# Kernel optimization log

Measured on AMD Instinct MI355X. Metric: run time of the kernel, lower is better.

Reference implementation:

```python
import jax, jax.numpy as jnp
import numpy as np

K = 3            # kernel_size
KK = K * K       # 9 neighbors per pixel
DILATIONS = [1, 2, 3]
NUM_HEADS = 3


def conv2d(x, w, b, dilation, padding):
    # x: [B,Cin,H,W], w: [Cout,Cin,kh,kw]
    out = jax.lax.conv_general_dilated(
        x, w, window_strides=(1, 1),
        padding=((padding, padding), (padding, padding)),
        rhs_dilation=(dilation, dilation),
        dimension_numbers=('NCHW', 'OIHW', 'NCHW'))
    if b is not None:
        out = out + b[None, :, None, None]
    return out


def unfold3(x, dil):
    # nn.Unfold(kernel=3, dilation=dil, padding=dil, stride=1): [B,C,H,W] -> [B, C*9, H*W]
    B, C, H, W = x.shape
    xp = jnp.pad(x, ((0, 0), (0, 0), (dil, dil), (dil, dil)))
    patches = [xp[:, :, i * dil:i * dil + H, j * dil:j * dil + W]
               for i in range(K) for j in range(K)]
    p = jnp.stack(patches, axis=2)          # [B,C,9,H,W] (channel-major like torch unfold)
    return p.reshape(B, C * KK, H * W)


def bilinear_sample(x, py, px):
    # x: [B,C,H,W]; py, px: [B,K2,H,W] float sample coords -> [B,C,K2,H,W]
    B, C, H, W = x.shape
    K2 = py.shape[1]
    y0 = jnp.floor(py); x0 = jnp.floor(px)
    wy = py - y0; wx = px - x0
    x_flat = x.reshape(B, C, H * W)

    def gather(yi, xi):
        yii = yi.astype(jnp.int32); xii = xi.astype(jnp.int32)
        valid = (yii >= 0) & (yii < H) & (xii >= 0) & (xii < W)
        yc = jnp.clip(yii, 0, H - 1); xc = jnp.clip(xii, 0, W - 1)
        idx = (yc * W + xc).reshape(B, -1)                       # [B, K2*H*W]
        vals = jnp.take_along_axis(x_flat, idx[:, None, :], axis=2)
        vals = vals.reshape(B, C, K2, H, W)
        return vals * valid[:, None].astype(x.dtype)

    v00 = gather(y0, x0); v01 = gather(y0, x0 + 1)
    v10 = gather(y0 + 1, x0); v11 = gather(y0 + 1, x0 + 1)
    wy = wy[:, None]; wx = wx[:, None]
    return (v00 * (1 - wy) * (1 - wx) + v01 * (1 - wy) * wx
            + v10 * wy * (1 - wx) + v11 * wy * wx)


def deform_conv(x, offsets, w, b, dil):
    # torchvision DeformConv2d, stride 1, padding=dil, dilation=dil, kernel 3
    B, C, H, W = x.shape
    off = offsets.reshape(B, KK, 2, H, W)                 # [..., (dy,dx), ...]
    ky, kx = jnp.meshgrid(jnp.arange(K), jnp.arange(K), indexing='ij')
    base_dy = (ky.reshape(KK) * dil - dil).astype(x.dtype)
    base_dx = (kx.reshape(KK) * dil - dil).astype(x.dtype)
    hh = jnp.arange(H, dtype=x.dtype); ww = jnp.arange(W, dtype=x.dtype)
    py = hh[None, None, :, None] + base_dy[None, :, None, None] + off[:, :, 0]
    px = ww[None, None, None, :] + base_dx[None, :, None, None] + off[:, :, 1]
    sampled = bilinear_sample(x, py, px)                  # [B,C,9,H,W]
    out = jnp.einsum('bckhw,ock->bohw', sampled, w.reshape(w.shape[0], C, KK))
    return out + b[None, :, None, None]


def adda_attention(q, k, v, head_dim, dil, deform_params):
    # q,k,v: [B,d,H,W] (already stop-gradiented)
    B, d, H, W = q.shape
    scale = head_dim ** -0.5
    if dil != 1:
        ow, ob, dw, db = deform_params
        offsets = conv2d(k, ow, ob, dil, dil)             # [B, 2*9, H, W]
        k = deform_conv(k, offsets, dw, db, dil)
        v = deform_conv(v, offsets, dw, db, dil)
    ku = unfold3(k, dil)                                  # [B, d*9, HW]
    vu = unfold3(v, dil)
    g = d // head_dim
    HW = H * W
    qh = q.reshape(B, g, head_dim, 1, HW).transpose(0, 1, 4, 3, 2)   # [B,g,HW,1,hd]
    kh = ku.reshape(B, g, head_dim, KK, HW).transpose(0, 1, 4, 2, 3) # [B,g,HW,hd,9]
    vh = vu.reshape(B, g, head_dim, KK, HW).transpose(0, 1, 4, 3, 2) # [B,g,HW,9,hd]
    attn = jax.nn.softmax((qh @ kh) * scale, axis=-1)                # [B,g,HW,1,9]
    o = attn @ vh                                                    # [B,g,HW,1,hd]
    return o.transpose(0, 2, 1, 3, 4).reshape(B, H, W, d)


def setup_inputs() -> dict:
    key = jax.random.key(0)
    ks = jax.random.split(key, 16)
    B, H, W, C = 8, 64, 64, 192
    hd = C // NUM_HEADS  # 64 == C // num_dilation
    inp = {
        'x': jax.random.normal(ks[0], (B, H, W, C), jnp.float32),
        'qkv_w': jax.random.normal(ks[1], (3 * C, C, 1, 1), jnp.float32) * 0.05,
        'proj_w': jax.random.normal(ks[2], (C, C), jnp.float32) * 0.05,
        'proj_b': jnp.zeros((C,), jnp.float32),
        'off_w2': jax.random.normal(ks[3], (2 * KK, hd, K, K), jnp.float32) * 0.01,
        'off_b2': jnp.zeros((2 * KK,), jnp.float32),
        'def_w2': jax.random.normal(ks[4], (hd, hd, K, K), jnp.float32) * 0.05,
        'def_b2': jnp.zeros((hd,), jnp.float32),
        'off_w3': jax.random.normal(ks[5], (2 * KK, hd, K, K), jnp.float32) * 0.01,
        'off_b3': jnp.zeros((2 * KK,), jnp.float32),
        'def_w3': jax.random.normal(ks[6], (hd, hd, K, K), jnp.float32) * 0.05,
        'def_b3': jnp.zeros((hd,), jnp.float32),
    }
    return inp


def reference(x, qkv_w, proj_w, proj_b,
              off_w2, off_b2, def_w2, def_b2,
              off_w3, off_b3, def_w3, def_b3):
    B, H, W, C = x.shape
    nd = len(DILATIONS)
    d = C // nd
    hd = C // NUM_HEADS
    xc = x.transpose(0, 3, 1, 2)                              # [B,C,H,W]
    qkv = conv2d(xc, qkv_w, None, 1, 0)                       # [B,3C,H,W]
    qkv = qkv.reshape(B, 3, nd, d, H, W).transpose(2, 1, 0, 3, 4, 5)  # [nd,3,B,d,H,W]
    qkv = jax.lax.stop_gradient(qkv)                          # q,k,v are .detach()'d in torch
    deform = {2: (off_w2, off_b2, def_w2, def_b2),
              3: (off_w3, off_b3, def_w3, def_b3)}
    outs = []
    for i, dil in enumerate(DILATIONS):
        outs.append(adda_attention(qkv[i, 0], qkv[i, 1], qkv[i, 2],
                                   hd, dil, deform.get(dil)))
    out = jnp.stack(outs, axis=3).reshape(B, H, W, C)         # permute(1,2,3,0,4).reshape
    return out @ proj_w.T + proj_b
```

## Files before the change

kernel.cpp:

```cpp
#include <hip/hip_runtime.h>
#include <cmath>

#define kB    8
#define kH    64
#define kW    64
#define kHW   4096
#define kC    192
#define kD    64
#define kM    (kB * kHW)
#define kNQKV 576

typedef unsigned short ushort_t;
typedef __attribute__((ext_vector_type(8))) short  s8v;
typedef __attribute__((ext_vector_type(4))) float  f4v;

__device__ inline unsigned short bf16r(float f) {
    union { float f; unsigned u; } v; v.f = f;
    unsigned u = v.u + 0x7FFFu + ((v.u >> 16) & 1u);
    return (unsigned short)(u >> 16);
}
__device__ inline float bfu(short s) {
    union { unsigned u; float f; } v;
    v.u = ((unsigned)(unsigned short)s) << 16;
    return v.f;
}

__global__ void cvt_bf16(const float* __restrict__ src, unsigned* __restrict__ dst, int n2) {
    int i = blockIdx.x * 256 + threadIdx.x;
    if (i >= n2) return;
    float2 f = ((const float2*)src)[i];
    dst[i] = (unsigned)bf16r(f.x) | ((unsigned)bf16r(f.y) << 16);
}

__global__ void prep_all(const float* __restrict__ qkv_w,
                         const float* __restrict__ proj_w,
                         const float* __restrict__ def_w2,
                         const float* __restrict__ def_w3,
                         const float* __restrict__ off_w2,
                         const float* __restrict__ off_w3,
                         ushort_t* __restrict__ awb,
                         ushort_t* __restrict__ pwbp,
                         ushort_t* __restrict__ dwtb2,
                         ushort_t* __restrict__ dwtb3,
                         ushort_t* __restrict__ owtb2,
                         ushort_t* __restrict__ owtb3) {
    const int bid = blockIdx.x;
    const int tid = threadIdx.x;
    if (bid < 54) {
        int idx = bid * 256 + tid;
        if (idx >= 36 * 6 * 64) return;
        int lane = idx & 63;
        int kc   = (idx >> 6) % 6;
        int s    = idx / 384;
        int row  = s * 16 + (lane & 15);
        int k0   = kc * 32 + (lane >> 4) * 8;
        const float* src = qkv_w + (size_t)row * kC + k0;
        ushort_t* dst = awb + (size_t)idx * 8;
#pragma unroll
        for (int j = 0; j < 8; ++j) dst[j] = bf16r(src[j]);
    } else if (bid < 72) {
        int idx = (bid - 54) * 256 + tid;
        if (idx >= 12 * 6 * 64) return;
        int lane = idx & 63;
        int kc   = (idx >> 6) % 6;
        int s    = idx / 384;
        int row  = s * 16 + (lane & 15);
        int k0   = kc * 32 + (lane >> 4) * 8;
        const float* src = proj_w + (size_t)row * kC + k0;
        ushort_t* dst = pwbp + (size_t)idx * 8;
#pragma unroll
        for (int j = 0; j < 8; ++j) dst[j] = bf16r(src[j]);
    } else if (bid < 360) {
        const float* dw = (bid < 216) ? def_w2 : def_w3;
        ushort_t* dwtb  = (bid < 216) ? dwtb2 : dwtb3;
        int l = ((bid < 216) ? (bid - 72) : (bid - 216)) * 256 + tid;
        if (l >= kD * kD * 9) return;
        int o = l / 576;
        int c = (l / 9) % 64;
        int kk = l % 9;
        dwtb[(kk * 64 + o) * 64 + c] = bf16r(dw[l]);
    } else {
        const float* ow = (bid < 432) ? off_w2 : off_w3;
        ushort_t* owtb  = (bid < 432) ? owtb2 : owtb3;
        int l = ((bid < 432) ? (bid - 360) : (bid - 432)) * 256 + tid;
        if (l >= 9 * 32 * 64) return;
        int kk = l >> 11;
        int j  = (l >> 6) & 31;
        int c  = l & 63;
        owtb[l] = (j < 18) ? bf16r(ow[j * 576 + c * 9 + kk]) : (ushort_t)0;
    }
}

__global__ __launch_bounds__(256) void qkv_mfma3(const ushort_t* __restrict__ xb,
                                                 const ushort_t* __restrict__ awb,
                                                 ushort_t* __restrict__ qkvpx) {
    __shared__ ushort_t xs[64 * kC];

    const int tid = threadIdx.x;
    const int bx  = blockIdx.x;
    const int lb  = (bx & 7) * 64 + (bx >> 3);
    const int m0  = lb * 64;
    const int ty3 = blockIdx.y;

#pragma unroll
    for (int i = 0; i < 6; ++i) {
        int il = i * 256 + tid;
        int p  = il / 24;
        int cc = il % 24;
        uint4 v = *(const uint4*)(xb + (size_t)(m0 + p) * kC + cc * 8);
        int dst = p * 384 + ((cc * 16) ^ ((p & 7) << 4));
        *(uint4*)((char*)xs + dst) = v;
    }
    __syncthreads();

    const int lane = tid & 63;
    const int wave = tid >> 6;
    const int l15  = lane & 15;
    const int q    = lane >> 4;
    const int sbase = ty3 * 12 + wave * 3;

    f4v acc[3][4];
#pragma unroll
    for (int i = 0; i < 3; ++i)
#pragma unroll
        for (int m = 0; m < 4; ++m) acc[i][m] = (f4v){0.f, 0.f, 0.f, 0.f};

    const ushort_t* ap = awb + ((size_t)sbase * 6 * 64 + lane) * 8;

#pragma unroll
    for (int kc = 0; kc < 6; ++kc) {
        s8v bfr[4];
#pragma unroll
        for (int m = 0; m < 4; ++m) {
            int row = m * 16 + l15;
            int col = (kc * 64 + q * 16) ^ ((l15 & 7) << 4);
            bfr[m] = *(const s8v*)((const char*)xs + row * 384 + col);
        }
#pragma unroll
        for (int i = 0; i < 3; ++i) {
            s8v a = *(const s8v*)(ap + (size_t)(i * 6 + kc) * 64 * 8);
#pragma unroll
            for (int m = 0; m < 4; ++m)
                acc[i][m] = __builtin_amdgcn_mfma_f32_16x16x32_bf16(a, bfr[m], acc[i][m], 0, 0, 0);
        }
    }

#pragma unroll
    for (int i = 0; i < 3; ++i) {
        int s   = sbase + i;
        int ty  = s >> 2;
        int c64 = (s & 3) * 16 + q * 4;
        ushort_t* obase = qkvpx + (size_t)ty * kM * 64 + (size_t)m0 * 64 + c64;
#pragma unroll
        for (int m = 0; m < 4; ++m) {
            f4v v = acc[i][m];
            uint2 u;
            u.x = (unsigned)bf16r(v.x) | ((unsigned)bf16r(v.y) << 16);
            u.y = (unsigned)bf16r(v.z) | ((unsigned)bf16r(v.w) << 16);
            *(uint2*)(obase + (size_t)(m * 16 + l15) * 64) = u;
        }
    }
}

__global__ __launch_bounds__(256) void off_conv_mfma(const ushort_t* __restrict__ kpx,
                                                     const ushort_t* __restrict__ owtb,
                                                     const float* __restrict__ obias,
                                                     float* __restrict__ offb,
                                                     int dil) {
    const int lb = (blockIdx.x & 7) * 64 + (blockIdx.x >> 3);
    const int b = lb >> 6;
    const int y = lb & 63;
    const int tid  = threadIdx.x;
    const int lane = tid & 63;
    const int wave = tid >> 6;
    const int l15  = lane & 15;
    const int q    = lane >> 4;
    const int px   = wave * 16 + l15;

    const ushort_t* inpx = kpx + (size_t)b * kHW * 64 + q * 8;

    f4v acc[2];
    acc[0] = (f4v){0.f, 0.f, 0.f, 0.f};
    acc[1] = (f4v){0.f, 0.f, 0.f, 0.f};

#pragma unroll
    for (int kk = 0; kk < 9; ++kk) {
        const int yy = y + (kk / 3 - 1) * dil;
        const int xx = px + (kk % 3 - 1) * dil;
        const bool valid = (yy >= 0) & (yy < kH) & (xx >= 0) & (xx < kW);
        const size_t idx = valid ? (size_t)(yy * kW + xx) * 64 : 0;
        s8v a0 = *(const s8v*)(inpx + idx);
        s8v a1 = *(const s8v*)(inpx + idx + 32);
        if (!valid) {
            a0 = (s8v){0, 0, 0, 0, 0, 0, 0, 0};
            a1 = (s8v){0, 0, 0, 0, 0, 0, 0, 0};
        }
        const ushort_t* wb = owtb + (size_t)kk * 2048 + l15 * 64 + q * 8;
#pragma unroll
        for (int nbk = 0; nbk < 2; ++nbk) {
            s8v b0 = *(const s8v*)(wb + nbk * 1024);
            s8v b1 = *(const s8v*)(wb + nbk * 1024 + 32);
            acc[nbk] = __builtin_amdgcn_mfma_f32_16x16x32_bf16(a0, b0, acc[nbk], 0, 0, 0);
            acc[nbk] = __builtin_amdgcn_mfma_f32_16x16x32_bf16(a1, b1, acc[nbk], 0, 0, 0);
        }
    }
#pragma unroll
    for (int nbk = 0; nbk < 2; ++nbk) {
        int n = nbk * 16 + l15;
        if (n < 18) {
            float bias = obias[n];
            f4v v = acc[nbk];
            v.x += bias; v.y += bias; v.z += bias; v.w += bias;
            *(f4v*)&offb[((size_t)b * 18 + n) * kHW + y * kW + wave * 16 + q * 4] = v;
        }
    }
}

template<int DIL>
__global__ __launch_bounds__(512) void deform_lds(const ushort_t* __restrict__ kpx,
                                                  const ushort_t* __restrict__ vpx,
                                                  const float* __restrict__ offb,
                                                  const ushort_t* __restrict__ dwtb,
                                                  const float* __restrict__ db,
                                                  ushort_t* __restrict__ outkpx,
                                                  ushort_t* __restrict__ outvpx) {
    constexpr int NR = 2 * DIL + 4;
    __shared__ ushort_t kv[NR * 4096];
    __shared__ ushort_t wlds[9 * 4096];

    const int tid = threadIdx.x;
    const int bx  = blockIdx.x;
    const int lb  = (bx & 7) * 64 + (bx >> 3);
    const int t   = lb >> 8;
    const int b   = (lb >> 5) & 7;
    const int y0  = (lb & 31) * 2;
    const int wlo = y0 - DIL - 1;

    const ushort_t* inb = (t ? vpx : kpx) + (size_t)b * kHW * 64;
    ushort_t* outp = t ? outvpx : outkpx;

#pragma unroll
    for (int i = 0; i < 9; ++i) {
        int g = (i * 512 + tid) * 16;
        uint4 v = *(const uint4*)((const char*)dwtb + g);
        int row = (g >> 7) & 63;
        int dst = g ^ ((row & 7) << 4);
        *(uint4*)((char*)wlds + dst) = v;
    }
#pragma unroll
    for (int r = 0; r < NR; ++r) {
        int gy = min(max(wlo + r, 0), kH - 1);
        uint4 v = *(const uint4*)(inb + (size_t)gy * 4096 + tid * 8);
        int x  = tid >> 3;
        int cc = tid & 7;
        int dst = r * 8192 + ((x * 128 + cc * 16) ^ ((x & 7) << 4));
        *(uint4*)((char*)kv + dst) = v;
    }
    __syncthreads();

    const int lane = tid & 63;
    const int wave = tid >> 6;
    const int ry   = wave >> 2;
    const int wc   = wave & 3;
    const int l15  = lane & 15;
    const int q    = lane >> 4;
    const int y    = y0 + ry;
    const int px   = wc * 16 + l15;
    const int wsw  = (l15 & 7) << 4;
    const int wcol0 = (q * 16) ^ wsw;
    const int wcol1 = (q * 16 + 64) ^ wsw;

    const ushort_t* inpx = inb + q * 8;

    f4v acc[4];
#pragma unroll
    for (int ob = 0; ob < 4; ++ob) acc[ob] = (f4v){0.f, 0.f, 0.f, 0.f};

    const float* offrow = offb + (size_t)b * 18 * kHW + y * kW + px;
    float offv[18];
#pragma unroll
    for (int i = 0; i < 18; ++i) offv[i] = offrow[(size_t)i * kHW];

#pragma unroll
    for (int kk = 0; kk < 9; ++kk) {
        float oy = offv[kk * 2 + 0];
        float ox = offv[kk * 2 + 1];
        float py  = (float)y  + (float)((kk / 3 - 1) * DIL) + oy;
        float pxf = (float)px + (float)((kk % 3 - 1) * DIL) + ox;
        float fy = floorf(py), fx = floorf(pxf);
        float wy = py - fy, wx = pxf - fx;
        int iy0 = (int)fy, ix0 = (int)fx;
        int iy1 = iy0 + 1, ix1 = ix0 + 1;
        int y0c = min(max(iy0, 0), kH - 1), x0c = min(max(ix0, 0), kW - 1);
        int y1c = min(max(iy1, 0), kH - 1), x1c = min(max(ix1, 0), kW - 1);
        bool vy0 = (iy0 >= 0) & (iy0 < kH), vx0 = (ix0 >= 0) & (ix0 < kW);
        bool vy1 = (iy1 >= 0) & (iy1 < kH), vx1 = (ix1 >= 0) & (ix1 < kW);
        float w0 = (vy0 && vx0) ? (1.f - wy) * (1.f - wx) : 0.f;
        float w1 = (vy0 && vx1) ? (1.f - wy) * wx : 0.f;
        float w2 = (vy1 && vx0) ? wy * (1.f - wx) : 0.f;
        float w3 = (vy1 && vx1) ? wy * wx : 0.f;

        s8v c[8];
        if (__builtin_expect(fabsf(oy) < 1.0f, 1)) {
            int r0 = min(max(y0c - wlo, 0), NR - 1);
            int r1 = min(max(y1c - wlo, 0), NR - 1);
            int b00 = r0 * 8192 + ((x0c * 128 + q * 16) ^ ((x0c & 7) << 4));
            int b00h = r0 * 8192 + ((x0c * 128 + q * 16 + 64) ^ ((x0c & 7) << 4));
            int b01 = r0 * 8192 + ((x1c * 128 + q * 16) ^ ((x1c & 7) << 4));
            int b01h = r0 * 8192 + ((x1c * 128 + q * 16 + 64) ^ ((x1c & 7) << 4));
            int b10 = r1 * 8192 + ((x0c * 128 + q * 16) ^ ((x0c & 7) << 4));
            int b10h = r1 * 8192 + ((x0c * 128 + q * 16 + 64) ^ ((x0c & 7) << 4));
            int b11 = r1 * 8192 + ((x1c * 128 + q * 16) ^ ((x1c & 7) << 4));
            int b11h = r1 * 8192 + ((x1c * 128 + q * 16 + 64) ^ ((x1c & 7) << 4));
            c[0] = *(const s8v*)((const char*)kv + b00);
            c[1] = *(const s8v*)((const char*)kv + b00h);
            c[2] = *(const s8v*)((const char*)kv + b01);
            c[3] = *(const s8v*)((const char*)kv + b01h);
            c[4] = *(const s8v*)((const char*)kv + b10);
            c[5] = *(const s8v*)((const char*)kv + b10h);
            c[6] = *(const s8v*)((const char*)kv + b11);
            c[7] = *(const s8v*)((const char*)kv + b11h);
        } else {
            size_t i00 = (size_t)(y0c * kW + x0c) * 64;
            size_t i01 = (size_t)(y0c * kW + x1c) * 64;
            size_t i10 = (size_t)(y1c * kW + x0c) * 64;
            size_t i11 = (size_t)(y1c * kW + x1c) * 64;
            c[0] = *(const s8v*)(inpx + i00);
            c[1] = *(const s8v*)(inpx + i00 + 32);
            c[2] = *(const s8v*)(inpx + i01);
            c[3] = *(const s8v*)(inpx + i01 + 32);
            c[4] = *(const s8v*)(inpx + i10);
            c[5] = *(const s8v*)(inpx + i10 + 32);
            c[6] = *(const s8v*)(inpx + i11);
            c[7] = *(const s8v*)(inpx + i11 + 32);
        }

        s8v b0, b1;
#pragma unroll
        for (int j = 0; j < 8; ++j) {
            float v0 = w0 * bfu(c[0][j]) + w1 * bfu(c[2][j]) +
                       w2 * bfu(c[4][j]) + w3 * bfu(c[6][j]);
            float v1 = w0 * bfu(c[1][j]) + w1 * bfu(c[3][j]) +
                       w2 * bfu(c[5][j]) + w3 * bfu(c[7][j]);
            b0[j] = (short)bf16r(v0);
            b1[j] = (short)bf16r(v1);
        }
        const char* wkk = (const char*)wlds + kk * 8192 + l15 * 128;
#pragma unroll
        for (int obb = 0; obb < 4; ++obb) {
            s8v a0w = *(const s8v*)(wkk + obb * 2048 + wcol0);
            s8v a1w = *(const s8v*)(wkk + obb * 2048 + wcol1);
            acc[obb] = __builtin_amdgcn_mfma_f32_16x16x32_bf16(a0w, b0, acc[obb], 0, 0, 0);
            acc[obb] = __builtin_amdgcn_mfma_f32_16x16x32_bf16(a1w, b1, acc[obb], 0, 0, 0);
        }
    }

    ushort_t* orow = outp + ((size_t)b * kHW + y * kW + px) * 64 + q * 4;
#pragma unroll
    for (int obb = 0; obb < 4; ++obb) {
        float4 bias = *(const float4*)&db[obb * 16 + q * 4];
        f4v v = acc[obb];
        uint2 u;
        u.x = (unsigned)bf16r(v.x + bias.x) | ((unsigned)bf16r(v.y + bias.y) << 16);
        u.y = (unsigned)bf16r(v.z + bias.z) | ((unsigned)bf16r(v.w + bias.w) << 16);
        *(uint2*)(orow + obb * 16) = u;
    }
}

__global__ __launch_bounds__(256) void attn_px(const ushort_t* __restrict__ qpx,
                                               const ushort_t* __restrict__ kpx,
                                               const ushort_t* __restrict__ vpx,
                                               ushort_t* __restrict__ aopx,
                                               int branch, int dil) {
    const int lb = (blockIdx.x & 7) * 128 + (blockIdx.x >> 3);
    const int b    = lb >> 7;
    const int y    = (lb >> 1) & 63;
    const int half = lb & 1;
    const int tid  = threadIdx.x;
    const int wave = tid >> 6;
    const int l    = tid & 63;
    const int pxq  = l >> 3;
    const int cg   = l & 7;
    const int x = half * 32 + wave * 8 + pxq;
    const int p = y * kW + x;
    const size_t pbase = (size_t)b * kHW;

    const ushort_t* qb = qpx + (pbase + p) * 64 + cg * 8;
    s8v q0 = *(const s8v*)qb;
    float qf[8];
#pragma unroll
    for (int j = 0; j < 8; ++j) qf[j] = bfu(q0[j]);

    int offs[9]; float msk[9];
#pragma unroll
    for (int kk = 0; kk < 9; ++kk) {
        int dy = (kk / 3 - 1) * dil, dx = (kk % 3 - 1) * dil;
        int yy = y + dy, xx = x + dx;
        bool v = (yy >= 0) & (yy < kH) & (xx >= 0) & (xx < kW);
        offs[kk] = v ? (p + dy * kW + dx) : p;
        msk[kk] = v ? 1.f : 0.f;
    }
    float e[9];
#pragma unroll
    for (int kk = 0; kk < 9; ++kk) {
        const ushort_t* kp = kpx + (pbase + offs[kk]) * 64 + cg * 8;
        s8v k0 = *(const s8v*)kp;
        float s = 0.f;
#pragma unroll
        for (int j = 0; j < 8; ++j) s += qf[j] * bfu(k0[j]);
        s += __shfl_xor(s, 1);
        s += __shfl_xor(s, 2);
        s += __shfl_xor(s, 4);
        e[kk] = s * 0.125f * msk[kk];
    }
    float mx = -1e30f;
#pragma unroll
    for (int kk = 0; kk < 9; ++kk) mx = fmaxf(mx, e[kk]);
    float ssum = 0.f;
#pragma unroll
    for (int kk = 0; kk < 9; ++kk) { e[kk] = __expf(e[kk] - mx); ssum += e[kk]; }
    float inv = 1.f / ssum;
#pragma unroll
    for (int kk = 0; kk < 9; ++kk) e[kk] = e[kk] * inv * msk[kk];

    float acc[8];
#pragma unroll
    for (int j = 0; j < 8; ++j) acc[j] = 0.f;
#pragma unroll
    for (int kk = 0; kk < 9; ++kk) {
        const ushort_t* vp = vpx + (pbase + offs[kk]) * 64 + cg * 8;
        s8v v0 = *(const s8v*)vp;
        float w = e[kk];
#pragma unroll
        for (int j = 0; j < 8; ++j) acc[j] += w * bfu(v0[j]);
    }
    unsigned u[4];
#pragma unroll
    for (int i = 0; i < 4; ++i)
        u[i] = (unsigned)bf16r(acc[2 * i]) | ((unsigned)bf16r(acc[2 * i + 1]) << 16);
    ushort_t* ob = aopx + (pbase + p) * kC + branch * 64 + cg * 8;
    *(uint4*)ob = make_uint4(u[0], u[1], u[2], u[3]);
}

__global__ __launch_bounds__(256) void proj_mfma3(const ushort_t* __restrict__ aopx,
                                                  const ushort_t* __restrict__ pwbp,
                                                  const float* __restrict__ pb,
                                                  float* __restrict__ out) {
    __shared__ ushort_t xs[64 * kC];

    const int tid = threadIdx.x;
    const int bx  = blockIdx.x;
    const int lb  = (bx & 7) * 64 + (bx >> 3);
    const int m0  = lb * 64;

#pragma unroll
    for (int i = 0; i < 6; ++i) {
        int il = i * 256 + tid;
        int p  = il / 24;
        int cc = il % 24;
        uint4 v = *(const uint4*)(aopx + (size_t)(m0 + p) * kC + cc * 8);
        int dst = p * 384 + ((cc * 16) ^ ((p & 7) << 4));
        *(uint4*)((char*)xs + dst) = v;
    }
    __syncthreads();

    const int lane = tid & 63;
    const int wave = tid >> 6;
    const int l15  = lane & 15;
    const int q    = lane >> 4;
    const int sbase = wave * 3;

    f4v acc[3][4];
#pragma unroll
    for (int i = 0; i < 3; ++i)
#pragma unroll
        for (int m = 0; m < 4; ++m) acc[i][m] = (f4v){0.f, 0.f, 0.f, 0.f};

    const ushort_t* ap = pwbp + ((size_t)sbase * 6 * 64 + lane) * 8;

#pragma unroll
    for (int kc = 0; kc < 6; ++kc) {
        s8v bfr[4];
#pragma unroll
        for (int m = 0; m < 4; ++m) {
            int row = m * 16 + l15;
            int col = (kc * 64 + q * 16) ^ ((l15 & 7) << 4);
            bfr[m] = *(const s8v*)((const char*)xs + row * 384 + col);
        }
#pragma unroll
        for (int i = 0; i < 3; ++i) {
            s8v a = *(const s8v*)(ap + (size_t)(i * 6 + kc) * 64 * 8);
#pragma unroll
            for (int m = 0; m < 4; ++m)
                acc[i][m] = __builtin_amdgcn_mfma_f32_16x16x32_bf16(a, bfr[m], acc[i][m], 0, 0, 0);
        }
    }

#pragma unroll
    for (int i = 0; i < 3; ++i) {
        int s  = sbase + i;
        int n0 = s * 16 + q * 4;
        float4 bias = *(const float4*)&pb[n0];
#pragma unroll
        for (int m = 0; m < 4; ++m) {
            f4v v = acc[i][m];
            v.x += bias.x; v.y += bias.y; v.z += bias.z; v.w += bias.w;
            *(f4v*)&out[(size_t)(m0 + m * 16 + l15) * kC + n0] = v;
        }
    }
}

extern "C" void kernel_launch(void* const* d_in, const int* in_sizes, int n_in,
                              void* d_out, int out_size, void* d_ws, size_t ws_size,
                              hipStream_t stream) {
    const float* x      = (const float*)d_in[0];
    const float* qkv_w  = (const float*)d_in[1];
    const float* proj_w = (const float*)d_in[2];
    const float* proj_b = (const float*)d_in[3];
    const float* off_w2 = (const float*)d_in[4];
    const float* off_b2 = (const float*)d_in[5];
    const float* def_w2 = (const float*)d_in[6];
    const float* def_b2 = (const float*)d_in[7];
    const float* off_w3 = (const float*)d_in[8];
    const float* off_b3 = (const float*)d_in[9];
    const float* def_w3 = (const float*)d_in[10];
    const float* def_b3 = (const float*)d_in[11];
    float* out = (float*)d_out;

    float* ws   = (float*)d_ws;
    float* offb = ws;
    ushort_t* us = (ushort_t*)(offb + (size_t)18 * kM);
    ushort_t* xb     = us;  us += (size_t)kM * kC;
    ushort_t* qkvpx  = us;  us += (size_t)9 * kM * 64;
    ushort_t* kdpx   = us;  us += (size_t)kM * 64;
    ushort_t* vdpx   = us;  us += (size_t)kM * 64;
    ushort_t* aopx   = us;  us += (size_t)kM * kC;
    ushort_t* awb    = us;  us += (size_t)kNQKV * kC;
    ushort_t* pwbp   = us;  us += (size_t)kC * kC;
    ushort_t* dwtb2  = us;  us += kD * kD * 9;
    ushort_t* dwtb3  = us;  us += kD * kD * 9;
    ushort_t* owtb2  = us;  us += 9 * 32 * 64;
    ushort_t* owtb3  = us;  us += 9 * 32 * 64;

    cvt_bf16<<<(kM * kC / 2 + 255) / 256, 256, 0, stream>>>(x, (unsigned*)xb, kM * kC / 2);
    prep_all<<<504, 256, 0, stream>>>(qkv_w, proj_w, def_w2, def_w3, off_w2, off_w3,
                                      awb, pwbp, dwtb2, dwtb3, owtb2, owtb3);

    ushort_t* q0 = qkvpx;
    ushort_t* q1 = qkvpx + (size_t)1 * kM * 64;
    ushort_t* q2 = qkvpx + (size_t)2 * kM * 64;
    ushort_t* k0 = qkvpx + (size_t)3 * kM * 64;
    ushort_t* k1 = qkvpx + (size_t)4 * kM * 64;
    ushort_t* k2 = qkvpx + (size_t)5 * kM * 64;
    ushort_t* v0 = qkvpx + (size_t)6 * kM * 64;
    ushort_t* v1 = qkvpx + (size_t)7 * kM * 64;
    ushort_t* v2 = qkvpx + (size_t)8 * kM * 64;

    qkv_mfma3<<<dim3(kM / 64, 3), 256, 0, stream>>>(xb, awb, qkvpx);

    attn_px<<<kB * kH * 2, 256, 0, stream>>>(q0, k0, v0, aopx, 0, 1);

    off_conv_mfma<<<512, 256, 0, stream>>>(k1, owtb2, off_b2, offb, 2);
    deform_lds<2><<<512, 512, 0, stream>>>(k1, v1, offb, dwtb2, def_b2, kdpx, vdpx);
    attn_px<<<kB * kH * 2, 256, 0, stream>>>(q1, kdpx, vdpx, aopx, 1, 2);

    off_conv_mfma<<<512, 256, 0, stream>>>(k2, owtb3, off_b3, offb, 3);
    deform_lds<3><<<512, 512, 0, stream>>>(k2, v2, offb, dwtb3, def_b3, kdpx, vdpx);
    attn_px<<<kB * kH * 2, 256, 0, stream>>>(q2, kdpx, vdpx, aopx, 2, 3);

    proj_mfma3<<<512, 256, 0, stream>>>(aopx, pwbp, proj_b, out);
}
```

Measured before the change: 231.1 us.

## Stage K/V row windows in swizzled LDS for neighborhood attention

Replaces the per-pixel global-gather attention kernel with a templated version. Each 512-thread block processes two image rows and first copies the needed K and V rows (2*DIL+2 rows, clamped at the borders) into XOR-swizzled shared memory. The 9-neighbor dot products and weighted sums then read from LDS rather than re-reading global memory. Each thread now covers 16 channels instead of 8, which removes one shuffle stage. Shared memory use grows with dilation (up to 128KB for DIL=3), which cuts occupancy, and halo rows are loaded redundantly across blocks.

```diff
diff --git a/kernel.cpp b/kernel.cpp
--- a/kernel.cpp
+++ b/kernel.cpp
@@ -367,50 +367,85 @@
     }
 }
 
-__global__ __launch_bounds__(256) void attn_px(const ushort_t* __restrict__ qpx,
-                                               const ushort_t* __restrict__ kpx,
-                                               const ushort_t* __restrict__ vpx,
-                                               ushort_t* __restrict__ aopx,
-                                               int branch, int dil) {
-    const int lb = (blockIdx.x & 7) * 128 + (blockIdx.x >> 3);
-    const int b    = lb >> 7;
-    const int y    = (lb >> 1) & 63;
-    const int half = lb & 1;
-    const int tid  = threadIdx.x;
+template<int DIL>
+__global__ __launch_bounds__(512) void attn_lds(const ushort_t* __restrict__ qpx,
+                                                const ushort_t* __restrict__ kpx,
+                                                const ushort_t* __restrict__ vpx,
+                                                ushort_t* __restrict__ aopx,
+                                                int branch) {
+    constexpr int NR = 2 * DIL + 2;
+    __shared__ ushort_t ks[NR * 4096];
+    __shared__ ushort_t vs[NR * 4096];
+
+    const int tid = threadIdx.x;
+    const int bx  = blockIdx.x;
+    const int lb  = (bx & 7) * 32 + (bx >> 3);
+    const int b   = lb >> 5;
+    const int y0  = (lb & 31) * 2;
+    const int wlo = y0 - DIL;
+
+    const size_t pbase = (size_t)b * kHW;
+    const ushort_t* kb = kpx + pbase * 64;
+    const ushort_t* vb = vpx + pbase * 64;
+
+    {
+        int x  = tid >> 3;
+        int cc = tid & 7;
+        int dstc = (x * 128 + cc * 16) ^ ((x & 7) << 4);
+#pragma unroll
+        for (int r = 0; r < NR; ++r) {
+            int gy = min(max(wlo + r, 0), kH - 1);
+            *(uint4*)((char*)ks + r * 8192 + dstc) = *(const uint4*)(kb + (size_t)gy * 4096 + tid * 8);
+            *(uint4*)((char*)vs + r * 8192 + dstc) = *(const uint4*)(vb + (size_t)gy * 4096 + tid * 8);
+        }
+    }
+    __syncthreads();
+
     const int wave = tid >> 6;
     const int l    = tid & 63;
-    const int pxq  = l >> 3;
-    const int cg   = l & 7;
-    const int x = half * 32 + wave * 8 + pxq;
-    const int p = y * kW + x;
-    const size_t pbase = (size_t)b * kHW;
-
-    const ushort_t* qb = qpx + (pbase + p) * 64 + cg * 8;
+    const int ry   = wave >> 2;
+    const int wc   = wave & 3;
+    const int pxq  = l >> 2;
+    const int cg   = l & 3;
+    const int y  = y0 + ry;
+    const int x_ = wc * 16 + pxq;
+    const int p  = y * kW + x_;
+
+    const ushort_t* qb = qpx + (pbase + p) * 64 + cg * 16;
     s8v q0 = *(const s8v*)qb;
-    float qf[8];
-#pragma unroll
-    for (int j = 0; j < 8; ++j) qf[j] = bfu(q0[j]);
-
-    int offs[9]; float msk[9];
+    s8v q1 = *(const s8v*)(qb + 8);
+    float qf[16];
+#pragma unroll
+    for (int j = 0; j < 8; ++j) { qf[j] = bfu(q0[j]); qf[8 + j] = bfu(q1[j]); }
+
+    int a0s[9], a1s[9];
+    float msk[9];
 #pragma unroll
     for (int kk = 0; kk < 9; ++kk) {
-        int dy = (kk / 3 - 1) * dil, dx = (kk % 3 - 1) * dil;
-        int yy = y + dy, xx = x + dx;
+        int dy = (kk / 3 - 1) * DIL, dx = (kk % 3 - 1) * DIL;
+        int yy = y + dy, xx = x_ + dx;
         bool v = (yy >= 0) & (yy < kH) & (xx >= 0) & (xx < kW);
-        offs[kk] = v ? (p + dy * kW + dx) : p;
         msk[kk] = v ? 1.f : 0.f;
-    }
+        int r  = min(max(yy - wlo, 0), NR - 1);
+        int xc = min(max(xx, 0), kW - 1);
+        int sw = (xc & 7) << 4;
+        a0s[kk] = r * 8192 + ((xc * 128 + cg * 32) ^ sw);
+        a1s[kk] = r * 8192 + ((xc * 128 + cg * 32 + 16) ^ sw);
+    }
+
     float e[9];
 #pragma unroll
     for (int kk = 0; kk < 9; ++kk) {
-        const ushort_t* kp = kpx + (pbase + offs[kk]) * 64 + cg * 8;
-        s8v k0 = *(const s8v*)kp;
+        s8v k0 = *(const s8v*)((const char*)ks + a0s[kk]);
+        s8v k1 = *(const s8v*)((const char*)ks + a1s[kk]);
         float s = 0.f;
 #pragma unroll
-        for (int j = 0; j < 8; ++j) s += qf[j] * bfu(k0[j]);
+        for (int j = 0; j < 8; ++j) {
+            s += qf[j] * bfu(k0[j]);
+            s += qf[8 + j] * bfu(k1[j]);
+        }
         s += __shfl_xor(s, 1);
         s += __shfl_xor(s, 2);
-        s += __shfl_xor(s, 4);
         e[kk] = s * 0.125f * msk[kk];
     }
     float mx = -1e30f;
@@ -423,23 +458,27 @@
 #pragma unroll
     for (int kk = 0; kk < 9; ++kk) e[kk] = e[kk] * inv * msk[kk];
 
-    float acc[8];
-#pragma unroll
-    for (int j = 0; j < 8; ++j) acc[j] = 0.f;
+    float acc[16];
+#pragma unroll
+    for (int j = 0; j < 16; ++j) acc[j] = 0.f;
 #pragma unroll
     for (int kk = 0; kk < 9; ++kk) {
-        const ushort_t* vp = vpx + (pbase + offs[kk]) * 64 + cg * 8;
-        s8v v0 = *(const s8v*)vp;
+        s8v v0 = *(const s8v*)((const char*)vs + a0s[kk]);
+        s8v v1 = *(const s8v*)((const char*)vs + a1s[kk]);
         float w = e[kk];
 #pragma unroll
-        for (int j = 0; j < 8; ++j) acc[j] += w * bfu(v0[j]);
-    }
-    unsigned u[4];
-#pragma unroll
-    for (int i = 0; i < 4; ++i)
+        for (int j = 0; j < 8; ++j) {
+            acc[j] += w * bfu(v0[j]);
+            acc[8 + j] += w * bfu(v1[j]);
+        }
+    }
+    unsigned u[8];
+#pragma unroll
+    for (int i = 0; i < 8; ++i)
         u[i] = (unsigned)bf16r(acc[2 * i]) | ((unsigned)bf16r(acc[2 * i + 1]) << 16);
-    ushort_t* ob = aopx + (pbase + p) * kC + branch * 64 + cg * 8;
+    ushort_t* ob = aopx + (pbase + p) * kC + branch * 64 + cg * 16;
     *(uint4*)ob = make_uint4(u[0], u[1], u[2], u[3]);
+    *(uint4*)(ob + 8) = make_uint4(u[4], u[5], u[6], u[7]);
 }
 
 __global__ __launch_bounds__(256) void proj_mfma3(const ushort_t* __restrict__ aopx,
@@ -558,15 +597,15 @@
 
     qkv_mfma3<<<dim3(kM / 64, 3), 256, 0, stream>>>(xb, awb, qkvpx);
 
-    attn_px<<<kB * kH * 2, 256, 0, stream>>>(q0, k0, v0, aopx, 0, 1);
+    attn_lds<1><<<kB * kH / 2, 512, 0, stream>>>(q0, k0, v0, aopx, 0);
 
     off_conv_mfma<<<512, 256, 0, stream>>>(k1, owtb2, off_b2, offb, 2);
     deform_lds<2><<<512, 512, 0, stream>>>(k1, v1, offb, dwtb2, def_b2, kdpx, vdpx);
-    attn_px<<<kB * kH * 2, 256, 0, stream>>>(q1, kdpx, vdpx, aopx, 1, 2);
+    attn_lds<2><<<kB * kH / 2, 512, 0, stream>>>(q1, kdpx, vdpx, aopx, 1);
 
     off_conv_mfma<<<512, 256, 0, stream>>>(k2, owtb3, off_b3, offb, 3);
     deform_lds<3><<<512, 512, 0, stream>>>(k2, v2, offb, dwtb3, def_b3, kdpx, vdpx);
-    attn_px<<<kB * kH * 2, 256, 0, stream>>>(q2, kdpx, vdpx, aopx, 2, 3);
+    attn_lds<3><<<kB * kH / 2, 512, 0, stream>>>(q2, kdpx, vdpx, aopx, 2);
 
     proj_mfma3<<<512, 256, 0, stream>>>(aopx, pwbp, proj_b, out);
 }
```

Measured after the change: 229.5 us. No clear change (-0.7%).
